# Performance work log

Measured on AMD Instinct MI355X. Metric: run time of the kernel, lower is better.

Reference implementation:

```python
import jax, jax.numpy as jnp
import numpy as np

B, N, C, H = 8, 1024, 384, 6
D = C // H
SPAN = C  # att_span = pos_ebd_size = dim (module sets max_relative_positions = dim)
SCALE_FACTOR = 3  # 1 + c2p + p2c


def setup_inputs() -> dict:
    key = jax.random.key(0)
    ks = jax.random.split(key, 10)
    w = lambda k, shp: jax.random.normal(k, shp, jnp.float32) * 0.02
    rel_pos = (jnp.arange(N)[:, None] - jnp.arange(N)[None, :]).astype(jnp.int32)
    return {
        "x": jax.random.normal(ks[0], (B, N, C), jnp.float32),
        "relative_pos": rel_pos,
        "rel_embeddings": jax.random.normal(ks[1], (2 * SPAN, C), jnp.float32) * 0.02,
        "Wq": w(ks[2], (C, C)), "bq": jnp.zeros((C,), jnp.float32),
        "Wk": w(ks[3], (C, C)), "bk": jnp.zeros((C,), jnp.float32),
        "Wv": w(ks[4], (C, C)), "bv": jnp.zeros((C,), jnp.float32),
        "Wpk": w(ks[5], (C, C)), "bpk": jnp.zeros((C,), jnp.float32),
        "Wpq": w(ks[6], (C, C)), "bpq": jnp.zeros((C,), jnp.float32),
        "Wo": w(ks[7], (C, C)), "bo": jnp.zeros((C,), jnp.float32),
    }


def reference(x, relative_pos, rel_embeddings, Wq, bq, Wk, bk, Wv, bv,
              Wpk, bpk, Wpq, bpq, Wo, bo):
    Bx, Nx, Cx = x.shape
    # content projections -> (B, H, N, D)
    q = (x @ Wq + bq).reshape(Bx, Nx, H, D).transpose(0, 2, 1, 3)
    k = (x @ Wk + bk).reshape(Bx, Nx, H, D).transpose(0, 2, 1, 3)
    v = (x @ Wv + bv).reshape(Bx, Nx, H, D).transpose(0, 2, 1, 3)
    scale = jnp.sqrt(jnp.asarray(D * SCALE_FACTOR, jnp.float32))
    attn = jnp.einsum('bhnd,bhmd->bhnm', q, k) / scale  # (B,H,N,N)

    # positional projections of rel_embeddings[0:2*SPAN] -> (H, 2*SPAN, D)
    pos_k = (rel_embeddings @ Wpk + bpk).reshape(2 * SPAN, H, D).transpose(1, 0, 2)
    pos_q = (rel_embeddings @ Wpq + bpq).reshape(2 * SPAN, H, D).transpose(1, 0, 2)

    rp = relative_pos.astype(jnp.int32)
    # content->position: gather columns of q @ pos_k^T by bucketed index
    c2p_pos = jnp.clip(rp + SPAN, 0, 2 * SPAN - 1)  # (N,N)
    c2p = jnp.einsum('bhnd,hpd->bhnp', q, pos_k)    # (B,H,N,2*SPAN)
    c2p = jnp.take_along_axis(
        c2p, jnp.broadcast_to(c2p_pos[None, None], (Bx, H, Nx, Nx)), axis=-1)

    # position->content: gather columns of k @ pos_q^T, then transpose
    p2c_pos = jnp.clip(-rp + SPAN, 0, 2 * SPAN - 1)
    p2c = jnp.einsum('bhnd,hpd->bhnp', k, pos_q)    # (B,H,N,2*SPAN)
    p2c = jnp.take_along_axis(
        p2c, jnp.broadcast_to(p2c_pos[None, None], (Bx, H, Nx, Nx)), axis=-1)
    p2c = jnp.swapaxes(p2c, -1, -2)

    attn = attn + (c2p + p2c) / scale
    probs = jax.nn.softmax(attn, axis=-1)
    out = jnp.einsum('bhnm,bhmd->bhnd', probs, v)
    out = out.transpose(0, 2, 1, 3).reshape(Bx, Nx, Cx)
    return out @ Wo + bo
```

## Files before the change

kernel.cpp:

```cpp
#include <hip/hip_runtime.h>
#include <math.h>

typedef __attribute__((ext_vector_type(8))) short short8;
typedef __attribute__((ext_vector_type(4))) float v4f;
typedef __attribute__((ext_vector_type(4))) unsigned short us4;

#define INV_SCALE 0.07216878364870322f

__device__ __forceinline__ unsigned short f2bf(float f) {
  unsigned u = __builtin_bit_cast(unsigned, f);
  u = (u + 0x7FFFu + ((u >> 16) & 1u)) >> 16;
  return (unsigned short)u;
}
__device__ __forceinline__ float bf2f(unsigned short h) {
  unsigned u = ((unsigned)h) << 16;
  return __builtin_bit_cast(float, u);
}

enum { OM_PLAIN = 0, OM_Q = 1, OM_K = 2, OM_VT = 3, OM_PK = 4, OM_PQ = 5 };

__global__ __launch_bounds__(256) void transpose_w(
    const float* __restrict__ Wq, const float* __restrict__ Wk,
    const float* __restrict__ Wv, const float* __restrict__ Wpk,
    const float* __restrict__ Wpq, const float* __restrict__ Wo,
    unsigned short* __restrict__ Wt) {
  __shared__ unsigned short Ts[64][68];
  const int mat = blockIdx.y;
  const float* W = mat == 0 ? Wq : mat == 1 ? Wk : mat == 2 ? Wv
                 : mat == 3 ? Wpk : mat == 4 ? Wpq : Wo;
  const int tk = (blockIdx.x % 6) * 64, tn = (blockIdx.x / 6) * 64;
  const int t = threadIdx.x;
#pragma unroll
  for (int it = 0; it < 4; ++it) {
    int r = (t >> 4) + it * 16, c = (t & 15) * 4;
    float4 v = *(const float4*)(W + (size_t)(tk + r) * 384 + tn + c);
    us4 p = {f2bf(v.x), f2bf(v.y), f2bf(v.z), f2bf(v.w)};
    *(us4*)&Ts[r][c] = p;
  }
  __syncthreads();
  unsigned short* out = Wt + (size_t)mat * 147456;
#pragma unroll
  for (int it = 0; it < 2; ++it) {
    int n = (t >> 3) + it * 32, kc = (t & 7) * 8;
    unsigned short tmp[8];
#pragma unroll
    for (int j = 0; j < 8; ++j) tmp[j] = Ts[kc + j][n];
    *(short8*)(out + (size_t)(tn + n) * 384 + tk + kc) = *(short8*)tmp;
  }
}

template <typename AT, int OMODE>
__device__ __forceinline__ void pgemm_body(
    const AT* __restrict__ A, const unsigned short* __restrict__ Bt,
    const float* __restrict__ bias, void* __restrict__ out,
    int m0, int n0, float scale, unsigned short (*Bs)[392]) {
  const int t = threadIdx.x;
  const int lane = t & 63, w = t >> 6, li = lane & 15, quad = lane >> 4;

  {
    int r = t >> 2, cq = (t & 3) * 96;
#pragma unroll
    for (int i = 0; i < 12; ++i)
      *(short8*)&Bs[r][cq + i * 8] =
          *(const short8*)(Bt + (size_t)(n0 + r) * 384 + cq + i * 8);
  }
  const int row = m0 + w * 16 + li;
  short8 afr[12];
#pragma unroll
  for (int kk = 0; kk < 12; ++kk) {
    if constexpr (sizeof(AT) == 4) {
      float4 u0 = *(const float4*)((const float*)A + (size_t)row * 384 + kk * 32 + quad * 8);
      float4 u1 = *(const float4*)((const float*)A + (size_t)row * 384 + kk * 32 + quad * 8 + 4);
      short8 v;
      v[0] = (short)f2bf(u0.x); v[1] = (short)f2bf(u0.y);
      v[2] = (short)f2bf(u0.z); v[3] = (short)f2bf(u0.w);
      v[4] = (short)f2bf(u1.x); v[5] = (short)f2bf(u1.y);
      v[6] = (short)f2bf(u1.z); v[7] = (short)f2bf(u1.w);
      afr[kk] = v;
    } else {
      afr[kk] = *(const short8*)((const unsigned short*)A + (size_t)row * 384 + kk * 32 + quad * 8);
    }
  }
  __syncthreads();

  v4f acc[4] = {};
#pragma unroll
  for (int kk = 0; kk < 12; ++kk) {
#pragma unroll
    for (int nt = 0; nt < 4; ++nt) {
      short8 bf = *(const short8*)&Bs[nt * 16 + li][kk * 32 + quad * 8];
      acc[nt] = __builtin_amdgcn_mfma_f32_16x16x32_bf16(afr[kk], bf, acc[nt], 0, 0, 0);
    }
  }

#pragma unroll
  for (int nt = 0; nt < 4; ++nt) {
    int col = n0 + nt * 16 + li;
    float bv = bias[col];
    int h = col >> 6, d = col & 63;
#pragma unroll
    for (int i = 0; i < 4; ++i) {
      int orow = m0 + w * 16 + quad * 4 + i;
      float val = (acc[nt][i] + bv) * scale;
      if constexpr (OMODE == OM_PLAIN) {
        ((float*)out)[(size_t)orow * 384 + col] = val;
      } else if constexpr (OMODE == OM_Q || OMODE == OM_K) {
        int b = orow >> 10, n = orow & 1023;
        ((unsigned short*)out)[((size_t)(b * 6 + h) << 16) + (n << 6) + d] = f2bf(val);
      } else if constexpr (OMODE == OM_VT) {
        int b = orow >> 10, n = orow & 1023;
        ((unsigned short*)out)[((size_t)(b * 6 + h) << 16) + (d << 10) + n] = f2bf(val);
      } else {
        ((unsigned short*)out)[(size_t)h * 49152 + (size_t)orow * 64 + d] = f2bf(val);
      }
    }
  }
}

__global__ __launch_bounds__(256, 3) void proj_all(
    const float* __restrict__ x, const float* __restrict__ re,
    const unsigned short* __restrict__ Wt,
    const float* __restrict__ bq, const float* __restrict__ bk,
    const float* __restrict__ bv, const float* __restrict__ bpk,
    const float* __restrict__ bpq,
    unsigned short* __restrict__ qw, unsigned short* __restrict__ kw,
    unsigned short* __restrict__ vtw, unsigned short* __restrict__ pkw,
    unsigned short* __restrict__ pqw) {
  __shared__ __align__(16) unsigned short Bs[64][392];
  const int which = blockIdx.y / 6;
  const int n0 = (blockIdx.y % 6) * 64;
  const int m0 = blockIdx.x * 64;
  if (which >= 3 && m0 >= 768) return;
  const float* A = which < 3 ? x : re;
  const unsigned short* Bt = Wt + (size_t)which * 147456;
  switch (which) {
    case 0: pgemm_body<float, OM_Q >(A, Bt, bq,  qw,  m0, n0, INV_SCALE, Bs); break;
    case 1: pgemm_body<float, OM_K >(A, Bt, bk,  kw,  m0, n0, 1.f, Bs); break;
    case 2: pgemm_body<float, OM_VT>(A, Bt, bv,  vtw, m0, n0, 1.f, Bs); break;
    case 3: pgemm_body<float, OM_PK>(A, Bt, bpk, pkw, m0, n0, 1.f, Bs); break;
    default: pgemm_body<float, OM_PQ>(A, Bt, bpq, pqw, m0, n0, INV_SCALE, Bs); break;
  }
}

__global__ __launch_bounds__(256, 3) void out_gemm(
    const unsigned short* __restrict__ ao, const unsigned short* __restrict__ Bt,
    const float* __restrict__ bo, float* __restrict__ out) {
  __shared__ __align__(16) unsigned short Bs[64][392];
  pgemm_body<unsigned short, OM_PLAIN>(ao, Bt, bo, out,
                                       blockIdx.x * 64, blockIdx.y * 64, 1.f, Bs);
}

#define ASTR 72

__global__ __launch_bounds__(256, 3) void attn_fused(
    const unsigned short* __restrict__ q, const unsigned short* __restrict__ k,
    const unsigned short* __restrict__ vt, const unsigned short* __restrict__ pk,
    const unsigned short* __restrict__ pq, unsigned short* __restrict__ ao) {
  __shared__ __align__(16) unsigned short band1[128][ASTR];
  __shared__ __align__(16) unsigned short band2[128][ASTR];
  __shared__ __align__(16) unsigned short Ps[64][ASTR];

  const int bh = blockIdx.y;
  const int h = bh % 6, b = bh / 6;
  const int n0 = blockIdx.x * 64;
  const int t = threadIdx.x;
  const int lane = t & 63, w = t >> 6;
  const int li = lane & 15, quad = lane >> 4;

  const unsigned short* qb = q + ((size_t)bh << 16);
  const unsigned short* kb = k + ((size_t)bh << 16);
  const unsigned short* vb = vt + ((size_t)bh << 16);
  const unsigned short* pkh = pk + (size_t)h * 49152;
  const unsigned short* pqh = pq + (size_t)h * 49152;

  short8 aq0 = *(const short8*)(qb + (size_t)(n0 + w * 16 + li) * 64 + quad * 8);
  short8 aq1 = *(const short8*)(qb + (size_t)(n0 + w * 16 + li) * 64 + 32 + quad * 8);

  float l_part[4] = {0.f, 0.f, 0.f, 0.f};
  v4f o[4] = {};

  for (int j0 = 0; j0 < 1024; j0 += 64) {
    __syncthreads();
    {
      const int pb = n0 - j0 - 63 + 384;
      int r = t >> 1, c = (t & 1) * 32;
      int src = pb + r;
      src = src < 0 ? 0 : (src > 767 ? 767 : src);
      const unsigned short* p1 = pkh + (size_t)src * 64 + c;
      const unsigned short* p2 = pqh + (size_t)src * 64 + c;
#pragma unroll
      for (int s = 0; s < 4; ++s) {
        *(short8*)&band1[r][c + s * 8] = *(const short8*)(p1 + s * 8);
        *(short8*)&band2[r][c + s * 8] = *(const short8*)(p2 + s * 8);
      }
    }
    __syncthreads();

    short8 ak0 = *(const short8*)(kb + (size_t)(j0 + w * 16 + li) * 64 + quad * 8);
    short8 ak1 = *(const short8*)(kb + (size_t)(j0 + w * 16 + li) * 64 + 32 + quad * 8);

    v4f t1a[8] = {}, t2a[8] = {};
#pragma unroll
    for (int ct = 0; ct < 8; ++ct) {
      short8 b10 = *(const short8*)&band1[ct * 16 + li][quad * 8];
      short8 b11 = *(const short8*)&band1[ct * 16 + li][32 + quad * 8];
      t1a[ct] = __builtin_amdgcn_mfma_f32_16x16x32_bf16(aq0, b10, t1a[ct], 0, 0, 0);
      t1a[ct] = __builtin_amdgcn_mfma_f32_16x16x32_bf16(aq1, b11, t1a[ct], 0, 0, 0);
      short8 b20 = *(const short8*)&band2[ct * 16 + li][quad * 8];
      short8 b21 = *(const short8*)&band2[ct * 16 + li][32 + quad * 8];
      t2a[ct] = __builtin_amdgcn_mfma_f32_16x16x32_bf16(ak0, b20, t2a[ct], 0, 0, 0);
      t2a[ct] = __builtin_amdgcn_mfma_f32_16x16x32_bf16(ak1, b21, t2a[ct], 0, 0, 0);
    }
    __syncthreads();

#pragma unroll
    for (int ct = 0; ct < 8; ++ct) {
      us4 p1 = {f2bf(t1a[ct][0]), f2bf(t1a[ct][1]), f2bf(t1a[ct][2]), f2bf(t1a[ct][3])};
      us4 p2 = {f2bf(t2a[ct][0]), f2bf(t2a[ct][1]), f2bf(t2a[ct][2]), f2bf(t2a[ct][3])};
      *(us4*)&band1[ct * 16 + li][w * 16 + quad * 4] = p1;
      *(us4*)&band2[ct * 16 + li][w * 16 + quad * 4] = p2;
    }
    v4f sqk[4] = {};
#pragma unroll
    for (int nt = 0; nt < 4; ++nt) {
      short8 b0 = *(const short8*)(kb + (size_t)(j0 + nt * 16 + li) * 64 + quad * 8);
      short8 b1 = *(const short8*)(kb + (size_t)(j0 + nt * 16 + li) * 64 + 32 + quad * 8);
      sqk[nt] = __builtin_amdgcn_mfma_f32_16x16x32_bf16(aq0, b0, sqk[nt], 0, 0, 0);
      sqk[nt] = __builtin_amdgcn_mfma_f32_16x16x32_bf16(aq1, b1, sqk[nt], 0, 0, 0);
    }
    __syncthreads();

#pragma unroll
    for (int nt = 0; nt < 4; ++nt) {
      int jl = nt * 16 + li;
#pragma unroll
      for (int i = 0; i < 4; ++i) {
        int nl = w * 16 + quad * 4 + i;
        int r = nl - jl + 63;
        float s = sqk[nt][i] + bf2f(band1[r][nl]) + bf2f(band2[r][jl]);
        float p = __expf(s);
        l_part[i] += p;
        Ps[nl][jl] = f2bf(p);
      }
    }
#pragma unroll
    for (int kst = 0; kst < 2; ++kst) {
      short8 ap = *(const short8*)&Ps[w * 16 + li][kst * 32 + quad * 8];
#pragma unroll
      for (int nt = 0; nt < 4; ++nt) {
        short8 bv2 = *(const short8*)(vb + (size_t)(nt * 16 + li) * 1024 + j0 + kst * 32 + quad * 8);
        o[nt] = __builtin_amdgcn_mfma_f32_16x16x32_bf16(ap, bv2, o[nt], 0, 0, 0);
      }
    }
  }

#pragma unroll
  for (int i = 0; i < 4; ++i) {
    float l = l_part[i];
    l += __shfl_xor(l, 1);
    l += __shfl_xor(l, 2);
    l += __shfl_xor(l, 4);
    l += __shfl_xor(l, 8);
    float inv_l = 1.f / l;
    int nl = w * 16 + quad * 4 + i;
#pragma unroll
    for (int nt = 0; nt < 4; ++nt)
      ao[((size_t)(b * 1024 + n0 + nl)) * 384 + h * 64 + nt * 16 + li] =
          f2bf(o[nt][i] * inv_l);
  }
}

extern "C" void kernel_launch(void* const* d_in, const int* in_sizes, int n_in,
                              void* d_out, int out_size, void* d_ws,
                              size_t ws_size, hipStream_t stream) {
  const float* x   = (const float*)d_in[0];
  const float* re  = (const float*)d_in[2];
  const float* Wq  = (const float*)d_in[3];
  const float* bq  = (const float*)d_in[4];
  const float* Wk  = (const float*)d_in[5];
  const float* bk  = (const float*)d_in[6];
  const float* Wv  = (const float*)d_in[7];
  const float* bv  = (const float*)d_in[8];
  const float* Wpk = (const float*)d_in[9];
  const float* bpk = (const float*)d_in[10];
  const float* Wpq = (const float*)d_in[11];
  const float* bpq = (const float*)d_in[12];
  const float* Wo  = (const float*)d_in[13];
  const float* bo  = (const float*)d_in[14];
  float* out = (float*)d_out;

  unsigned short* ws = (unsigned short*)d_ws;
  unsigned short* Wt  = ws;
  unsigned short* qw  = Wt + 884736;
  unsigned short* kw  = qw + 3145728;
  unsigned short* vtw = kw + 3145728;
  unsigned short* pkw = vtw + 3145728;
  unsigned short* pqw = pkw + 294912;
  unsigned short* aow = pqw + 294912;

  transpose_w<<<dim3(36, 6), 256, 0, stream>>>(Wq, Wk, Wv, Wpk, Wpq, Wo, Wt);
  proj_all<<<dim3(128, 30), 256, 0, stream>>>(x, re, Wt, bq, bk, bv, bpk, bpq,
                                              qw, kw, vtw, pkw, pqw);
  attn_fused<<<dim3(16, 48), 256, 0, stream>>>(qw, kw, vtw, pkw, pqw, aow);
  out_gemm<<<dim3(128, 6), 256, 0, stream>>>(aow, Wt + 5 * 147456, bo, out);
}
```

Baseline: 275.3 us.

## Compute positional bands from register-held Q/K fragments with swizzled LDS

Each wave now keeps Q fragments for all 64 query rows and K fragments for the current key tile in registers. It reads pos_k/pos_q rows straight from global memory and computes its own slice of the c2p/p2c bands, so the band no longer has to be staged in LDS and then overwritten. This removes one or two barriers per iteration and the separate staging copy. The QK^T product reuses the K fragments already held in registers. LDS arrays drop their padding and use an XOR swizzle to avoid bank conflicts. The cost is more registers (16 short8 fragments), which may hurt occupancy at 3 blocks per CU, and duplicated global loads of Q and K across waves.

```diff
diff --git a/kernel.cpp b/kernel.cpp
--- a/kernel.cpp
+++ b/kernel.cpp
@@ -150,15 +150,15 @@
                                        blockIdx.x * 64, blockIdx.y * 64, 1.f, Bs);
 }
 
-#define ASTR 72
+#define BSW(r, c) ((c) ^ (((r) & 7) << 3))
 
 __global__ __launch_bounds__(256, 3) void attn_fused(
     const unsigned short* __restrict__ q, const unsigned short* __restrict__ k,
     const unsigned short* __restrict__ vt, const unsigned short* __restrict__ pk,
     const unsigned short* __restrict__ pq, unsigned short* __restrict__ ao) {
-  __shared__ __align__(16) unsigned short band1[128][ASTR];
-  __shared__ __align__(16) unsigned short band2[128][ASTR];
-  __shared__ __align__(16) unsigned short Ps[64][ASTR];
+  __shared__ __align__(16) unsigned short band1[128][64];
+  __shared__ __align__(16) unsigned short band2[128][64];
+  __shared__ __align__(16) unsigned short Ps[64][64];
 
   const int bh = blockIdx.y;
   const int h = bh % 6, b = bh / 6;
@@ -173,60 +173,72 @@
   const unsigned short* pkh = pk + (size_t)h * 49152;
   const unsigned short* pqh = pq + (size_t)h * 49152;
 
-  short8 aq0 = *(const short8*)(qb + (size_t)(n0 + w * 16 + li) * 64 + quad * 8);
-  short8 aq1 = *(const short8*)(qb + (size_t)(n0 + w * 16 + li) * 64 + 32 + quad * 8);
+  short8 qfr[8];
+#pragma unroll
+  for (int rg = 0; rg < 4; ++rg) {
+    qfr[rg * 2 + 0] = *(const short8*)(qb + (size_t)(n0 + rg * 16 + li) * 64 + quad * 8);
+    qfr[rg * 2 + 1] = *(const short8*)(qb + (size_t)(n0 + rg * 16 + li) * 64 + 32 + quad * 8);
+  }
 
   float l_part[4] = {0.f, 0.f, 0.f, 0.f};
   v4f o[4] = {};
 
   for (int j0 = 0; j0 < 1024; j0 += 64) {
     __syncthreads();
-    {
-      const int pb = n0 - j0 - 63 + 384;
-      int r = t >> 1, c = (t & 1) * 32;
-      int src = pb + r;
+    const int pb = n0 - j0 + 321;
+
+#pragma unroll
+    for (int c2 = 0; c2 < 2; ++c2) {
+      const int br = w * 32 + c2 * 16 + li;
+      int src = pb + br;
       src = src < 0 ? 0 : (src > 767 ? 767 : src);
-      const unsigned short* p1 = pkh + (size_t)src * 64 + c;
-      const unsigned short* p2 = pqh + (size_t)src * 64 + c;
-#pragma unroll
-      for (int s = 0; s < 4; ++s) {
-        *(short8*)&band1[r][c + s * 8] = *(const short8*)(p1 + s * 8);
-        *(short8*)&band2[r][c + s * 8] = *(const short8*)(p2 + s * 8);
-      }
-    }
-    __syncthreads();
-
-    short8 ak0 = *(const short8*)(kb + (size_t)(j0 + w * 16 + li) * 64 + quad * 8);
-    short8 ak1 = *(const short8*)(kb + (size_t)(j0 + w * 16 + li) * 64 + 32 + quad * 8);
-
-    v4f t1a[8] = {}, t2a[8] = {};
-#pragma unroll
-    for (int ct = 0; ct < 8; ++ct) {
-      short8 b10 = *(const short8*)&band1[ct * 16 + li][quad * 8];
-      short8 b11 = *(const short8*)&band1[ct * 16 + li][32 + quad * 8];
-      t1a[ct] = __builtin_amdgcn_mfma_f32_16x16x32_bf16(aq0, b10, t1a[ct], 0, 0, 0);
-      t1a[ct] = __builtin_amdgcn_mfma_f32_16x16x32_bf16(aq1, b11, t1a[ct], 0, 0, 0);
-      short8 b20 = *(const short8*)&band2[ct * 16 + li][quad * 8];
-      short8 b21 = *(const short8*)&band2[ct * 16 + li][32 + quad * 8];
-      t2a[ct] = __builtin_amdgcn_mfma_f32_16x16x32_bf16(ak0, b20, t2a[ct], 0, 0, 0);
-      t2a[ct] = __builtin_amdgcn_mfma_f32_16x16x32_bf16(ak1, b21, t2a[ct], 0, 0, 0);
-    }
-    __syncthreads();
-
-#pragma unroll
-    for (int ct = 0; ct < 8; ++ct) {
-      us4 p1 = {f2bf(t1a[ct][0]), f2bf(t1a[ct][1]), f2bf(t1a[ct][2]), f2bf(t1a[ct][3])};
-      us4 p2 = {f2bf(t2a[ct][0]), f2bf(t2a[ct][1]), f2bf(t2a[ct][2]), f2bf(t2a[ct][3])};
-      *(us4*)&band1[ct * 16 + li][w * 16 + quad * 4] = p1;
-      *(us4*)&band2[ct * 16 + li][w * 16 + quad * 4] = p2;
-    }
+      short8 b0 = *(const short8*)(pkh + (size_t)src * 64 + quad * 8);
+      short8 b1 = *(const short8*)(pkh + (size_t)src * 64 + 32 + quad * 8);
+      v4f tt[4] = {};
+#pragma unroll
+      for (int rg = 0; rg < 4; ++rg) {
+        tt[rg] = __builtin_amdgcn_mfma_f32_16x16x32_bf16(qfr[rg * 2 + 0], b0, tt[rg], 0, 0, 0);
+        tt[rg] = __builtin_amdgcn_mfma_f32_16x16x32_bf16(qfr[rg * 2 + 1], b1, tt[rg], 0, 0, 0);
+      }
+#pragma unroll
+      for (int rg = 0; rg < 4; ++rg) {
+        us4 p = {f2bf(tt[rg][0]), f2bf(tt[rg][1]), f2bf(tt[rg][2]), f2bf(tt[rg][3])};
+        *(us4*)&band1[br][BSW(br, rg * 16 + quad * 4)] = p;
+      }
+    }
+
+    short8 kfr[8];
+#pragma unroll
+    for (int rg = 0; rg < 4; ++rg) {
+      kfr[rg * 2 + 0] = *(const short8*)(kb + (size_t)(j0 + rg * 16 + li) * 64 + quad * 8);
+      kfr[rg * 2 + 1] = *(const short8*)(kb + (size_t)(j0 + rg * 16 + li) * 64 + 32 + quad * 8);
+    }
+
+#pragma unroll
+    for (int c2 = 0; c2 < 2; ++c2) {
+      const int br = w * 32 + c2 * 16 + li;
+      int src = pb + br;
+      src = src < 0 ? 0 : (src > 767 ? 767 : src);
+      short8 b0 = *(const short8*)(pqh + (size_t)src * 64 + quad * 8);
+      short8 b1 = *(const short8*)(pqh + (size_t)src * 64 + 32 + quad * 8);
+      v4f tt[4] = {};
+#pragma unroll
+      for (int rg = 0; rg < 4; ++rg) {
+        tt[rg] = __builtin_amdgcn_mfma_f32_16x16x32_bf16(kfr[rg * 2 + 0], b0, tt[rg], 0, 0, 0);
+        tt[rg] = __builtin_amdgcn_mfma_f32_16x16x32_bf16(kfr[rg * 2 + 1], b1, tt[rg], 0, 0, 0);
+      }
+#pragma unroll
+      for (int rg = 0; rg < 4; ++rg) {
+        us4 p = {f2bf(tt[rg][0]), f2bf(tt[rg][1]), f2bf(tt[rg][2]), f2bf(tt[rg][3])};
+        *(us4*)&band2[br][BSW(br, rg * 16 + quad * 4)] = p;
+      }
+    }
+
     v4f sqk[4] = {};
 #pragma unroll
     for (int nt = 0; nt < 4; ++nt) {
-      short8 b0 = *(const short8*)(kb + (size_t)(j0 + nt * 16 + li) * 64 + quad * 8);
-      short8 b1 = *(const short8*)(kb + (size_t)(j0 + nt * 16 + li) * 64 + 32 + quad * 8);
-      sqk[nt] = __builtin_amdgcn_mfma_f32_16x16x32_bf16(aq0, b0, sqk[nt], 0, 0, 0);
-      sqk[nt] = __builtin_amdgcn_mfma_f32_16x16x32_bf16(aq1, b1, sqk[nt], 0, 0, 0);
+      sqk[nt] = __builtin_amdgcn_mfma_f32_16x16x32_bf16(qfr[w * 2 + 0], kfr[nt * 2 + 0], sqk[nt], 0, 0, 0);
+      sqk[nt] = __builtin_amdgcn_mfma_f32_16x16x32_bf16(qfr[w * 2 + 1], kfr[nt * 2 + 1], sqk[nt], 0, 0, 0);
     }
     __syncthreads();
 
@@ -237,15 +249,15 @@
       for (int i = 0; i < 4; ++i) {
         int nl = w * 16 + quad * 4 + i;
         int r = nl - jl + 63;
-        float s = sqk[nt][i] + bf2f(band1[r][nl]) + bf2f(band2[r][jl]);
+        float s = sqk[nt][i] + bf2f(band1[r][BSW(r, nl)]) + bf2f(band2[r][BSW(r, jl)]);
         float p = __expf(s);
         l_part[i] += p;
-        Ps[nl][jl] = f2bf(p);
+        Ps[nl][BSW(nl, jl)] = f2bf(p);
       }
     }
 #pragma unroll
     for (int kst = 0; kst < 2; ++kst) {
-      short8 ap = *(const short8*)&Ps[w * 16 + li][kst * 32 + quad * 8];
+      short8 ap = *(const short8*)&Ps[w * 16 + li][BSW(w * 16 + li, kst * 32 + quad * 8)];
 #pragma unroll
       for (int nt = 0; nt < 4; ++nt) {
         short8 bv2 = *(const short8*)(vb + (size_t)(nt * 16 + li) * 1024 + j0 + kst * 32 + quad * 8);
```

Result: slower. 335.6 us (+21.9%).

## Prefetch next positional band into registers and remap blocks for L2 locality

Applied to the files above, without the earlier changes.

Loads for the next iteration's pk/pq band are issued into registers right after the current band is stored to shared memory, so global latency overlaps with the MFMA work of the current tile. The block index is also remapped so that consecutive blocks are spread across batch-head groups in a chosen order, aiming at better cache locality or XCD distribution. The prefetch adds 32 VGPRs of staging, which may reduce occupancy under the 3-blocks launch bound, and the final iteration loads a band that is never used.

```diff
diff --git a/kernel.cpp b/kernel.cpp
--- a/kernel.cpp
+++ b/kernel.cpp
@@ -160,9 +160,11 @@
   __shared__ __align__(16) unsigned short band2[128][ASTR];
   __shared__ __align__(16) unsigned short Ps[64][ASTR];
 
-  const int bh = blockIdx.y;
+  const int f = blockIdx.x + (blockIdx.y << 4);
+  const int g = f & 7, s = f >> 3;
+  const int bh = g * 6 + (s >> 4);
+  const int n0 = (s & 15) * 64;
   const int h = bh % 6, b = bh / 6;
-  const int n0 = blockIdx.x * 64;
   const int t = threadIdx.x;
   const int lane = t & 63, w = t >> 6;
   const int li = lane & 15, quad = lane >> 4;
@@ -179,22 +181,40 @@
   float l_part[4] = {0.f, 0.f, 0.f, 0.f};
   v4f o[4] = {};
 
+  const int sr = t >> 1, sc = (t & 1) * 32;
+  short8 st1[4], st2[4];
+  {
+    int src = n0 - 0 - 63 + 384 + sr;
+    src = src < 0 ? 0 : (src > 767 ? 767 : src);
+    const unsigned short* p1 = pkh + (size_t)src * 64 + sc;
+    const unsigned short* p2 = pqh + (size_t)src * 64 + sc;
+#pragma unroll
+    for (int ss = 0; ss < 4; ++ss) {
+      st1[ss] = *(const short8*)(p1 + ss * 8);
+      st2[ss] = *(const short8*)(p2 + ss * 8);
+    }
+  }
+
   for (int j0 = 0; j0 < 1024; j0 += 64) {
     __syncthreads();
+#pragma unroll
+    for (int ss = 0; ss < 4; ++ss) {
+      *(short8*)&band1[sr][sc + ss * 8] = st1[ss];
+      *(short8*)&band2[sr][sc + ss * 8] = st2[ss];
+    }
+    __syncthreads();
+
     {
-      const int pb = n0 - j0 - 63 + 384;
-      int r = t >> 1, c = (t & 1) * 32;
-      int src = pb + r;
+      int src = n0 - (j0 + 64) - 63 + 384 + sr;
       src = src < 0 ? 0 : (src > 767 ? 767 : src);
-      const unsigned short* p1 = pkh + (size_t)src * 64 + c;
-      const unsigned short* p2 = pqh + (size_t)src * 64 + c;
-#pragma unroll
-      for (int s = 0; s < 4; ++s) {
-        *(short8*)&band1[r][c + s * 8] = *(const short8*)(p1 + s * 8);
-        *(short8*)&band2[r][c + s * 8] = *(const short8*)(p2 + s * 8);
+      const unsigned short* p1 = pkh + (size_t)src * 64 + sc;
+      const unsigned short* p2 = pqh + (size_t)src * 64 + sc;
+#pragma unroll
+      for (int ss = 0; ss < 4; ++ss) {
+        st1[ss] = *(const short8*)(p1 + ss * 8);
+        st2[ss] = *(const short8*)(p2 + ss * 8);
       }
     }
-    __syncthreads();
 
     short8 ak0 = *(const short8*)(kb + (size_t)(j0 + w * 16 + li) * 64 + quad * 8);
     short8 ak1 = *(const short8*)(kb + (size_t)(j0 + w * 16 + li) * 64 + 32 + quad * 8);
@@ -237,8 +257,8 @@
       for (int i = 0; i < 4; ++i) {
         int nl = w * 16 + quad * 4 + i;
         int r = nl - jl + 63;
-        float s = sqk[nt][i] + bf2f(band1[r][nl]) + bf2f(band2[r][jl]);
-        float p = __expf(s);
+        float s2 = sqk[nt][i] + bf2f(band1[r][nl]) + bf2f(band2[r][jl]);
+        float p = __expf(s2);
         l_part[i] += p;
         Ps[nl][jl] = f2bf(p);
       }
```

New measurement: 271.6 us. No clear change (-1.3%).
